# Kernel optimization log

Measured on AMD Instinct MI355X. Metric: run time of the kernel, lower is better.

The kernel has to match this reference:

```python
import jax, jax.numpy as jnp
import numpy as np

B, D, N_CAT, S = 8192, 128, 8192, 4
EPS = 1e-12  # F.normalize eps


def setup_inputs() -> dict:
    key = jax.random.key(0)
    k1, k2, k3, k4 = jax.random.split(key, 4)
    return {
        "batch_x": jax.random.normal(k1, (B, D), dtype=jnp.float32),
        "cat": jax.random.normal(k2, (N_CAT, D), dtype=jnp.float32),
        "y": jax.random.uniform(k3, (N_CAT,), dtype=jnp.float32),
        "phi": jax.random.normal(k4, (S, D), dtype=jnp.float32) * (6.0 / (D + 1)) ** 0.5,  # xavier-ish scale
        "bias": jnp.zeros((1,), dtype=jnp.float32),
    }


def reference(batch_x, cat, y, phi, bias):
    # con[n, b] = cat[n] . batch_x[b]   -> [N_cat, B]
    con = cat @ batch_x.T
    # F.normalize(con, p=4, dim=0): divide each column by its 4-norm (clamped)
    norm4 = jnp.sum(jnp.abs(con) ** 4, axis=0, keepdims=True) ** 0.25
    con = con / jnp.maximum(norm4, EPS)
    con = jax.nn.softmax(con, axis=0)
    s = phi.shape[0]
    c = con.shape[0] // s
    psi = con.reshape(s, c, con.shape[1])      # source_size chunks of [C, B]
    y_r = y.reshape(s, c)                      # source_size chunks of labels
    theta = jnp.exp(batch_x @ phi.T).T         # [S, B], raw exp (theta/sum_src unused in original)
    # sum over sources and chunk rows of y[s,c] * psi[s,c,b] * theta[s,b]
    y_hat = jnp.einsum('sc,scb,sb->b', y_r, psi, theta) + bias
    return y_hat
```

## Files before the change

kernel.cpp:

```cpp
#include <hip/hip_runtime.h>
#include <hip/hip_bf16.h>
#include <math.h>

typedef __bf16 bf16x8 __attribute__((ext_vector_type(8)));
typedef float f32x4 __attribute__((ext_vector_type(4)));

namespace {
constexpr int BN   = 8192;
constexpr int DK   = 128;
constexpr int NCAT = 8192;
constexpr int SRC  = 4;
constexpr int RG   = 16;
constexpr int TROWS = 64;
constexpr int NT   = 8;
constexpr float LOG2E = 1.4426950408889634f;
}

__device__ __forceinline__ float4 ld4(const float* p) {
    return *reinterpret_cast<const float4*>(p);
}

__device__ __forceinline__ void load_lds16(const unsigned short* g, unsigned short* l) {
    __builtin_amdgcn_global_load_lds(
        (const __attribute__((address_space(1))) void*)g,
        (__attribute__((address_space(3))) void*)l, 16, 0, 0);
}

__global__ __launch_bounds__(256) void k_convert2(const float* __restrict__ x,
                                                  const float* __restrict__ cat,
                                                  unsigned short* __restrict__ xb,
                                                  unsigned short* __restrict__ catb) {
    const int i = blockIdx.x * 256 + threadIdx.x;
    const int nx = BN * DK / 8;
    const float* src;
    unsigned short* dst;
    int j;
    size_t dchunk;
    if (i < nx) {
        src = x; dst = xb; j = i; dchunk = (size_t)j;
    } else {
        src = cat; dst = catb; j = i - nx;
        const int r = j >> 4, c = j & 15;
        const int rt = r >> 6, r6 = r & 63;
        dchunk = (size_t)rt * 1024 + r6 * 16 + (c ^ (r6 & 7));
    }
    const float4 a = ld4(src + (size_t)j * 8);
    const float4 b = ld4(src + (size_t)j * 8 + 4);
    float vals[8] = {a.x, a.y, a.z, a.w, b.x, b.y, b.z, b.w};
    union { unsigned short u[8]; uint4 v; } o;
#pragma unroll
    for (int q = 0; q < 8; ++q) {
        __hip_bfloat16 h = __float2bfloat16(vals[q]);
        o.u[q] = *reinterpret_cast<unsigned short*>(&h);
    }
    *reinterpret_cast<uint4*>(&dst[dchunk * 8]) = o.v;
}

template <int PASS>
__global__ __launch_bounds__(256, 4) void k_pass(
    const unsigned short* __restrict__ xb,
    const unsigned short* __restrict__ catb,
    const float* __restrict__ y,
    const float* __restrict__ pp4in,
    float* __restrict__ outA,
    float* __restrict__ outB) {
    __shared__ __align__(16) unsigned short As[2][TROWS * DK];
    __shared__ float ysh[512];
    __shared__ float nsh[128];

    const int t = threadIdx.x;
    const int colbase = blockIdx.x * 128;
    const int rowgrp = blockIdx.y;
    const int tile0 = rowgrp * NT;

    const int wid = t >> 6;
    const int lane = t & 63;
    const int lr = lane & 15;
    const int kb = lane >> 4;

#pragma unroll
    for (int q = 0; q < 4; ++q)
        load_lds16(catb + ((size_t)tile0 * 1024 + (wid * 4 + q) * 64 + lane) * 8,
                   &As[0][(wid * 4 + q) * 64 * 8]);

    bf16x8 Bf[2][4];
#pragma unroll
    for (int j = 0; j < 2; ++j)
#pragma unroll
        for (int kk = 0; kk < 4; ++kk)
            Bf[j][kk] = *reinterpret_cast<const bf16x8*>(
                &xb[(size_t)(colbase + wid * 32 + j * 16 + lr) * DK + kk * 32 + kb * 8]);

    if (PASS == 2) {
        if (t < 128) {
            float sp = 0.f;
#pragma unroll
            for (int r = 0; r < RG; ++r) sp += pp4in[r * BN + colbase + t];
            nsh[t] = LOG2E / fmaxf(sqrtf(sqrtf(sp)), 1e-12f);
        }
#pragma unroll
        for (int q = t; q < 512; q += 256) ysh[q] = y[rowgrp * 512 + q];
    }
    __syncthreads();

    float inm[2];
    if (PASS == 2) {
#pragma unroll
        for (int j = 0; j < 2; ++j) inm[j] = nsh[wid * 32 + j * 16 + lr];
    }

    float accA[2] = {0.f, 0.f};
    float accB[2] = {0.f, 0.f};

    for (int tl = 0; tl < NT; ++tl) {
        const int cur = tl & 1, nxt = cur ^ 1;
        if (tl < NT - 1) {
#pragma unroll
            for (int q = 0; q < 4; ++q)
                load_lds16(catb + ((size_t)(tile0 + tl + 1) * 1024 +
                                   (wid * 4 + q) * 64 + lane) * 8,
                           &As[nxt][(wid * 4 + q) * 64 * 8]);
        }

        f32x4 acc[4][2];
#pragma unroll
        for (int i = 0; i < 4; ++i)
#pragma unroll
            for (int j = 0; j < 2; ++j) acc[i][j] = (f32x4){0.f, 0.f, 0.f, 0.f};

#pragma unroll
        for (int kk = 0; kk < 4; ++kk) {
            bf16x8 a[4];
#pragma unroll
            for (int i = 0; i < 4; ++i) {
                const int row = i * 16 + lr;
                const int chunk = (kk * 4 + kb) ^ (lr & 7);
                a[i] = *reinterpret_cast<const bf16x8*>(&As[cur][row * 128 + chunk * 8]);
            }
#pragma unroll
            for (int i = 0; i < 4; ++i)
#pragma unroll
                for (int j = 0; j < 2; ++j)
                    acc[i][j] = __builtin_amdgcn_mfma_f32_16x16x32_bf16(
                        a[i], Bf[j][kk], acc[i][j], 0, 0, 0);
        }

        if (PASS == 1) {
#pragma unroll
            for (int i = 0; i < 4; ++i)
#pragma unroll
                for (int j = 0; j < 2; ++j)
#pragma unroll
                    for (int r = 0; r < 4; ++r) {
                        const float v = acc[i][j][r];
                        const float v2 = v * v;
                        accA[j] = fmaf(v2, v2, accA[j]);
                    }
        } else {
#pragma unroll
            for (int i = 0; i < 4; ++i) {
                const float4 yv =
                    *reinterpret_cast<const float4*>(&ysh[tl * 64 + i * 16 + kb * 4]);
                const float yr4[4] = {yv.x, yv.y, yv.z, yv.w};
#pragma unroll
                for (int r = 0; r < 4; ++r) {
                    const float yr = yr4[r];
#pragma unroll
                    for (int j = 0; j < 2; ++j) {
                        const float e = exp2f(acc[i][j][r] * inm[j]);
                        accA[j] += e;
                        accB[j] = fmaf(yr, e, accB[j]);
                    }
                }
            }
        }
        __syncthreads();
    }

#pragma unroll
    for (int j = 0; j < 2; ++j) {
        accA[j] += __shfl_xor(accA[j], 16, 64);
        accA[j] += __shfl_xor(accA[j], 32, 64);
        if (PASS == 2) {
            accB[j] += __shfl_xor(accB[j], 16, 64);
            accB[j] += __shfl_xor(accB[j], 32, 64);
        }
    }
    if (lane < 16) {
#pragma unroll
        for (int j = 0; j < 2; ++j) {
            const int col = colbase + wid * 32 + j * 16 + lane;
            outA[(size_t)rowgrp * BN + col] = accA[j];
            if (PASS == 2) outB[(size_t)rowgrp * BN + col] = accB[j];
        }
    }
}

__global__ __launch_bounds__(256) void k_final(const float* __restrict__ x,
                                               const float* __restrict__ phi,
                                               const float* __restrict__ pZ,
                                               const float* __restrict__ pW,
                                               const float* __restrict__ bias,
                                               float* __restrict__ out) {
    const int g = blockIdx.x * 256 + threadIdx.x;
    const int b = g >> 2, s = g & 3;
    float dot = 0.f;
#pragma unroll
    for (int k = 0; k < DK; k += 4) {
        const float4 xv = ld4(&x[(size_t)b * DK + k]);
        const float4 pv = ld4(&phi[s * DK + k]);
        dot += xv.x * pv.x + xv.y * pv.y + xv.z * pv.z + xv.w * pv.w;
    }
    float W = 0.f, Z = 0.f;
#pragma unroll
    for (int r = 0; r < 4; ++r) {
        W += pW[(size_t)(4 * s + r) * BN + b];
        Z += pZ[(size_t)(4 * s + r) * BN + b];
    }
    float v = __expf(dot) * W;
    v += __shfl_xor(v, 1, 64);
    v += __shfl_xor(v, 2, 64);
    Z += __shfl_xor(Z, 1, 64);
    Z += __shfl_xor(Z, 2, 64);
    if (s == 0) out[b] = v / Z + bias[0];
}

extern "C" void kernel_launch(void* const* d_in, const int* in_sizes, int n_in,
                              void* d_out, int out_size, void* d_ws, size_t ws_size,
                              hipStream_t stream) {
    const float* x    = (const float*)d_in[0];
    const float* cat  = (const float*)d_in[1];
    const float* y    = (const float*)d_in[2];
    const float* phi  = (const float*)d_in[3];
    const float* bias = (const float*)d_in[4];
    float* out = (float*)d_out;

    char* ws = (char*)d_ws;
    unsigned short* xb   = (unsigned short*)ws;
    unsigned short* catb = xb + (size_t)BN * DK;
    float* pp4 = (float*)(catb + (size_t)NCAT * DK);
    float* pZ  = pp4 + (size_t)RG * BN;
    float* pW  = pZ + (size_t)RG * BN;

    k_convert2<<<(BN * DK + NCAT * DK) / 8 / 256, 256, 0, stream>>>(x, cat, xb, catb);
    k_pass<1><<<dim3(BN / 128, RG), 256, 0, stream>>>(xb, catb, y, nullptr, pp4, nullptr);
    k_pass<2><<<dim3(BN / 128, RG), 256, 0, stream>>>(xb, catb, y, pp4, pZ, pW);
    k_final<<<BN * SRC / 256, 256, 0, stream>>>(x, phi, pZ, pW, bias, out);
}
```

Baseline: 64.98 us.

## Split cat rows across waves instead of columns, reduce partials via LDS

After: 87.22 us. +34.2%, slower.

```diff
diff --git a/kernel.cpp b/kernel.cpp
--- a/kernel.cpp
+++ b/kernel.cpp
@@ -57,7 +57,7 @@
 }
 
 template <int PASS>
-__global__ __launch_bounds__(256, 4) void k_pass(
+__global__ __launch_bounds__(256, 2) void k_pass(
     const unsigned short* __restrict__ xb,
     const unsigned short* __restrict__ catb,
     const float* __restrict__ y,
@@ -67,6 +67,8 @@
     __shared__ __align__(16) unsigned short As[2][TROWS * DK];
     __shared__ float ysh[512];
     __shared__ float nsh[128];
+    __shared__ float redA[4][128];
+    __shared__ float redB[4][128];
 
     const int t = threadIdx.x;
     const int colbase = blockIdx.x * 128;
@@ -83,13 +85,13 @@
         load_lds16(catb + ((size_t)tile0 * 1024 + (wid * 4 + q) * 64 + lane) * 8,
                    &As[0][(wid * 4 + q) * 64 * 8]);
 
-    bf16x8 Bf[2][4];
-#pragma unroll
-    for (int j = 0; j < 2; ++j)
+    bf16x8 Bf[8][4];
+#pragma unroll
+    for (int j = 0; j < 8; ++j)
 #pragma unroll
         for (int kk = 0; kk < 4; ++kk)
             Bf[j][kk] = *reinterpret_cast<const bf16x8*>(
-                &xb[(size_t)(colbase + wid * 32 + j * 16 + lr) * DK + kk * 32 + kb * 8]);
+                &xb[(size_t)(colbase + j * 16 + lr) * DK + kk * 32 + kb * 8]);
 
     if (PASS == 2) {
         if (t < 128) {
@@ -103,14 +105,14 @@
     }
     __syncthreads();
 
-    float inm[2];
+    float inm[8];
     if (PASS == 2) {
 #pragma unroll
-        for (int j = 0; j < 2; ++j) inm[j] = nsh[wid * 32 + j * 16 + lr];
-    }
-
-    float accA[2] = {0.f, 0.f};
-    float accB[2] = {0.f, 0.f};
+        for (int j = 0; j < 8; ++j) inm[j] = nsh[j * 16 + lr];
+    }
+
+    float accA[8] = {0.f, 0.f, 0.f, 0.f, 0.f, 0.f, 0.f, 0.f};
+    float accB[8] = {0.f, 0.f, 0.f, 0.f, 0.f, 0.f, 0.f, 0.f};
 
     for (int tl = 0; tl < NT; ++tl) {
         const int cur = tl & 1, nxt = cur ^ 1;
@@ -122,55 +124,43 @@
                            &As[nxt][(wid * 4 + q) * 64 * 8]);
         }
 
-        f32x4 acc[4][2];
-#pragma unroll
-        for (int i = 0; i < 4; ++i)
-#pragma unroll
-            for (int j = 0; j < 2; ++j) acc[i][j] = (f32x4){0.f, 0.f, 0.f, 0.f};
+        f32x4 acc[8];
+#pragma unroll
+        for (int j = 0; j < 8; ++j) acc[j] = (f32x4){0.f, 0.f, 0.f, 0.f};
 
 #pragma unroll
         for (int kk = 0; kk < 4; ++kk) {
-            bf16x8 a[4];
-#pragma unroll
-            for (int i = 0; i < 4; ++i) {
-                const int row = i * 16 + lr;
-                const int chunk = (kk * 4 + kb) ^ (lr & 7);
-                a[i] = *reinterpret_cast<const bf16x8*>(&As[cur][row * 128 + chunk * 8]);
-            }
-#pragma unroll
-            for (int i = 0; i < 4; ++i)
-#pragma unroll
-                for (int j = 0; j < 2; ++j)
-                    acc[i][j] = __builtin_amdgcn_mfma_f32_16x16x32_bf16(
-                        a[i], Bf[j][kk], acc[i][j], 0, 0, 0);
+            const int row = wid * 16 + lr;
+            const int chunk = (kk * 4 + kb) ^ (lr & 7);
+            const bf16x8 a =
+                *reinterpret_cast<const bf16x8*>(&As[cur][row * 128 + chunk * 8]);
+#pragma unroll
+            for (int j = 0; j < 8; ++j)
+                acc[j] = __builtin_amdgcn_mfma_f32_16x16x32_bf16(
+                    a, Bf[j][kk], acc[j], 0, 0, 0);
         }
 
         if (PASS == 1) {
 #pragma unroll
-            for (int i = 0; i < 4; ++i)
-#pragma unroll
-                for (int j = 0; j < 2; ++j)
-#pragma unroll
-                    for (int r = 0; r < 4; ++r) {
-                        const float v = acc[i][j][r];
-                        const float v2 = v * v;
-                        accA[j] = fmaf(v2, v2, accA[j]);
-                    }
+            for (int j = 0; j < 8; ++j)
+#pragma unroll
+                for (int r = 0; r < 4; ++r) {
+                    const float v = acc[j][r];
+                    const float v2 = v * v;
+                    accA[j] = fmaf(v2, v2, accA[j]);
+                }
         } else {
-#pragma unroll
-            for (int i = 0; i < 4; ++i) {
-                const float4 yv =
-                    *reinterpret_cast<const float4*>(&ysh[tl * 64 + i * 16 + kb * 4]);
-                const float yr4[4] = {yv.x, yv.y, yv.z, yv.w};
-#pragma unroll
-                for (int r = 0; r < 4; ++r) {
-                    const float yr = yr4[r];
-#pragma unroll
-                    for (int j = 0; j < 2; ++j) {
-                        const float e = exp2f(acc[i][j][r] * inm[j]);
-                        accA[j] += e;
-                        accB[j] = fmaf(yr, e, accB[j]);
-                    }
+            const float4 yv =
+                *reinterpret_cast<const float4*>(&ysh[tl * 64 + wid * 16 + kb * 4]);
+            const float yr4[4] = {yv.x, yv.y, yv.z, yv.w};
+#pragma unroll
+            for (int r = 0; r < 4; ++r) {
+                const float yr = yr4[r];
+#pragma unroll
+                for (int j = 0; j < 8; ++j) {
+                    const float e = exp2f(acc[j][r] * inm[j]);
+                    accA[j] += e;
+                    accB[j] = fmaf(yr, e, accB[j]);
                 }
             }
         }
@@ -178,7 +168,7 @@
     }
 
 #pragma unroll
-    for (int j = 0; j < 2; ++j) {
+    for (int j = 0; j < 8; ++j) {
         accA[j] += __shfl_xor(accA[j], 16, 64);
         accA[j] += __shfl_xor(accA[j], 32, 64);
         if (PASS == 2) {
@@ -188,11 +178,18 @@
     }
     if (lane < 16) {
 #pragma unroll
-        for (int j = 0; j < 2; ++j) {
-            const int col = colbase + wid * 32 + j * 16 + lane;
-            outA[(size_t)rowgrp * BN + col] = accA[j];
-            if (PASS == 2) outB[(size_t)rowgrp * BN + col] = accB[j];
-        }
+        for (int j = 0; j < 8; ++j) {
+            redA[wid][j * 16 + lane] = accA[j];
+            if (PASS == 2) redB[wid][j * 16 + lane] = accB[j];
+        }
+    }
+    __syncthreads();
+    if (t < 128) {
+        outA[(size_t)rowgrp * BN + colbase + t] =
+            redA[0][t] + redA[1][t] + redA[2][t] + redA[3][t];
+        if (PASS == 2)
+            outB[(size_t)rowgrp * BN + colbase + t] =
+                redB[0][t] + redB[1][t] + redB[2][t] + redB[3][t];
     }
 }
 
```
